# Optimization experiments

Measured on AMD Instinct MI355X. Metric: run time of the kernel, lower is better.

The kernel has to match this reference:

```python
import jax, jax.numpy as jnp
import numpy as np

NEAR, FAR, N_SAMPLES = 0.5, 2.5, 64


def setup_inputs() -> dict:
    key = jax.random.key(0)
    ks = jax.random.split(key, 12)
    N = 4096
    W = 256  # MLP width
    inp = {
        "rays_o": jax.random.normal(ks[0], (N, 3), jnp.float32),
        "rays_d": jax.random.normal(ks[1], (N, 3), jnp.float32),
        "t_rand": jax.random.uniform(ks[2], (N, N_SAMPLES), jnp.float32),
        "W1": jax.random.normal(ks[3], (3, W), jnp.float32) * 0.5,
        "b1": jnp.zeros((W,), jnp.float32),
        "W2": jax.random.normal(ks[4], (W, W), jnp.float32) * (1.0 / np.sqrt(W)),
        "b2": jnp.zeros((W,), jnp.float32),
        "W3": jax.random.normal(ks[5], (W, W), jnp.float32) * (1.0 / np.sqrt(W)),
        "b3": jnp.zeros((W,), jnp.float32),
        "Wd": jax.random.normal(ks[6], (W, 1), jnp.float32) * (1.0 / np.sqrt(W)),
        "bd": jnp.zeros((1,), jnp.float32),
        "W4": jax.random.normal(ks[7], (W + 3, 128), jnp.float32) * (1.0 / np.sqrt(W + 3)),
        "b4": jnp.zeros((128,), jnp.float32),
        "W5": jax.random.normal(ks[8], (128, 3), jnp.float32) * (1.0 / np.sqrt(128)),
        "b5": jnp.zeros((3,), jnp.float32),
    }
    return inp


def _nerf_mlp(pts, viewdirs, W1, b1, W2, b2, W3, b3, Wd, bd, W4, b4, W5, b5):
    # pts, viewdirs: [N, S, 3] -> rgb [N, S, 3], density [N, S]
    h = jax.nn.relu(pts @ W1 + b1)
    h = jax.nn.relu(h @ W2 + b2)
    h = jax.nn.relu(h @ W3 + b3)
    density = (h @ Wd + bd)[..., 0]
    h2 = jax.nn.relu(jnp.concatenate([h, viewdirs], axis=-1) @ W4 + b4)
    rgb = jax.nn.sigmoid(h2 @ W5 + b5)
    return rgb, density


def reference(rays_o, rays_d, t_rand, W1, b1, W2, b2, W3, b3, Wd, bd, W4, b4, W5, b5):
    N = rays_o.shape[0]
    # Stratified sampling along rays
    t_vals = jnp.linspace(0.0, 1.0, N_SAMPLES, dtype=jnp.float32)
    z = NEAR * (1.0 - t_vals) + FAR * t_vals                      # [S]
    z_vals = jnp.broadcast_to(z, (N, N_SAMPLES))
    mids = 0.5 * (z_vals[:, 1:] + z_vals[:, :-1])
    upper = jnp.concatenate([mids, z_vals[:, -1:]], axis=-1)
    lower = jnp.concatenate([z_vals[:, :1], mids], axis=-1)
    z_vals = lower + (upper - lower) * t_rand                      # [N, S]

    pts = rays_o[:, None, :] + rays_d[:, None, :] * z_vals[..., None]  # [N, S, 3]
    viewdirs = rays_d / (jnp.linalg.norm(rays_d, axis=-1, keepdims=True) + 1e-8)
    vdirs = jnp.broadcast_to(viewdirs[:, None, :], pts.shape)

    rgb, density = _nerf_mlp(pts, vdirs, W1, b1, W2, b2, W3, b3, Wd, bd, W4, b4, W5, b5)

    # Alpha compositing
    dists = z_vals[:, 1:] - z_vals[:, :-1]
    dists = jnp.concatenate([dists, jnp.full_like(dists[:, :1], 1e10)], axis=-1)
    alpha = 1.0 - jnp.exp(-jax.nn.relu(density) * dists)           # [N, S]
    trans = jnp.cumprod(
        jnp.concatenate([jnp.ones_like(alpha[:, :1]), 1.0 - alpha[:, :-1] + 1e-10], axis=-1),
        axis=-1,
    )
    weights = alpha * trans                                        # [N, S]
    rgb_map = jnp.sum(weights[..., None] * rgb, axis=-2)           # [N, 3]
    depth_map = jnp.sum(weights * z_vals, axis=-1)                 # [N]
    acc_map = jnp.sum(weights, axis=-1)                            # [N]
    rgb_map = rgb_map + (1.0 - acc_map[..., None])  # white background
    return rgb_map, depth_map, acc_map
```

## Files before the change

### kernel.cpp

```cpp
#include <hip/hip_runtime.h>
#include <stdint.h>


#define NRAYS 4096

typedef unsigned short u16;
typedef __attribute__((ext_vector_type(8))) short short8;
typedef __attribute__((ext_vector_type(4))) float f32x4;
typedef __attribute__((ext_vector_type(4))) unsigned int uint32x4;

__device__ __forceinline__ u16 f2bf(float f) {
  union { float f; uint32_t i; } v; v.f = f;
  return (u16)((v.i + 0x7FFFu + ((v.i >> 16) & 1u)) >> 16);
}
__device__ __forceinline__ float bf2f(u16 u) {
  union { uint32_t i; float f; } v; v.i = ((uint32_t)u) << 16; return v.f;
}
__device__ __forceinline__ uint32_t cvtpk(float lo, float hi) {
  uint32_t r;
  asm("v_cvt_pk_bf16_f32 %0, %1, %2" : "=v"(r) : "v"(lo), "v"(hi));
  return r;
}

__device__ __forceinline__ int fragidx(int n, int k) {
  return ((((n >> 4) * 8 + (k >> 5)) * 64 + ((k >> 3) & 3) * 16 + (n & 15)) << 3) + (k & 7);
}

__global__ void pack_weights(const float* __restrict__ W2, const float* __restrict__ W3,
                             const float* __restrict__ W4, u16* __restrict__ ws) {
  int idx = blockIdx.x * 256 + threadIdx.x;
  float v;
  int dst;
  if (idx < 65536) {
    int k = idx >> 8, n = idx & 255;
    v = W2[idx];
    dst = fragidx(n, k);
  } else if (idx < 131072) {
    int o = idx - 65536, k = o >> 8, n = o & 255;
    v = W3[o];
    dst = 65536 + fragidx(n, k);
  } else {
    int o = idx - 131072, k = o >> 7, n = o & 127;
    v = W4[o];
    dst = 131072 + fragidx(n, k);
  }
  ws[dst] = f2bf(v);
}

#define MFMA __builtin_amdgcn_mfma_f32_16x16x32_bf16
#define ZER4 (f32x4){0.f, 0.f, 0.f, 0.f}

#define KSTEP4(kq_, ACT) do {                                                \
    const int kq = (kq_);                                                    \
    short8 bv0 = *(const short8*)(bc0 + kq * 512);                           \
    short8 bv1 = *(const short8*)(bc1 + kq * 512);                           \
    short8 bv2 = *(const short8*)(bc2 + kq * 512);                           \
    short8 bv3 = *(const short8*)(bc3 + kq * 512);                           \
    const int sq = kq * 4 + quad;                                            \
    short8 av0 = *(const short8*)((ACT) + m0 * 256 + ((sq ^ (m0 & 31)) << 3)); \
    short8 av1 = *(const short8*)((ACT) + m1 * 256 + ((sq ^ (m1 & 31)) << 3)); \
    short8 av2 = *(const short8*)((ACT) + m2 * 256 + ((sq ^ (m2 & 31)) << 3)); \
    short8 av3 = *(const short8*)((ACT) + m3 * 256 + ((sq ^ (m3 & 31)) << 3)); \
    c00 = MFMA(av0, bv0, c00, 0, 0, 0); c10 = MFMA(av1, bv0, c10, 0, 0, 0);  \
    c20 = MFMA(av2, bv0, c20, 0, 0, 0); c30 = MFMA(av3, bv0, c30, 0, 0, 0);  \
    c01 = MFMA(av0, bv1, c01, 0, 0, 0); c11 = MFMA(av1, bv1, c11, 0, 0, 0);  \
    c21 = MFMA(av2, bv1, c21, 0, 0, 0); c31 = MFMA(av3, bv1, c31, 0, 0, 0);  \
    c02 = MFMA(av0, bv2, c02, 0, 0, 0); c12 = MFMA(av1, bv2, c12, 0, 0, 0);  \
    c22 = MFMA(av2, bv2, c22, 0, 0, 0); c32 = MFMA(av3, bv2, c32, 0, 0, 0);  \
    c03 = MFMA(av0, bv3, c03, 0, 0, 0); c13 = MFMA(av1, bv3, c13, 0, 0, 0);  \
    c23 = MFMA(av2, bv3, c23, 0, 0, 0); c33 = MFMA(av3, bv3, c33, 0, 0, 0);  \
  } while (0)

#define KSTEP2(kq_, ACT) do {                                                \
    const int kq = (kq_);                                                    \
    short8 bv0 = *(const short8*)(bc0 + kq * 512);                           \
    short8 bv1 = *(const short8*)(bc1 + kq * 512);                           \
    const int sq = kq * 4 + quad;                                            \
    short8 av0 = *(const short8*)((ACT) + m0 * 256 + ((sq ^ (m0 & 31)) << 3)); \
    short8 av1 = *(const short8*)((ACT) + m1 * 256 + ((sq ^ (m1 & 31)) << 3)); \
    short8 av2 = *(const short8*)((ACT) + m2 * 256 + ((sq ^ (m2 & 31)) << 3)); \
    short8 av3 = *(const short8*)((ACT) + m3 * 256 + ((sq ^ (m3 & 31)) << 3)); \
    c00 = MFMA(av0, bv0, c00, 0, 0, 0); c10 = MFMA(av1, bv0, c10, 0, 0, 0);  \
    c20 = MFMA(av2, bv0, c20, 0, 0, 0); c30 = MFMA(av3, bv0, c30, 0, 0, 0);  \
    c01 = MFMA(av0, bv1, c01, 0, 0, 0); c11 = MFMA(av1, bv1, c11, 0, 0, 0);  \
    c21 = MFMA(av2, bv1, c21, 0, 0, 0); c31 = MFMA(av3, bv1, c31, 0, 0, 0);  \
  } while (0)

#define EPIC(CV, mt, ng, addv, ACT) do {                                     \
    int su_ = ((ng) >> 3), so_ = ((ng) & 7);                                 \
    float f0_ = fmaxf((CV)[0] + (addv), 0.f);                                \
    float f1_ = fmaxf((CV)[1] + (addv), 0.f);                                \
    float f2_ = fmaxf((CV)[2] + (addv), 0.f);                                \
    float f3_ = fmaxf((CV)[3] + (addv), 0.f);                                \
    uint32_t p01_ = cvtpk(f0_, f1_), p23_ = cvtpk(f2_, f3_);                 \
    int mmb_ = (mt) * 16 + quad * 4;                                         \
    (ACT)[(mmb_ + 0) * 256 + ((su_ ^ ((mmb_ + 0) & 31)) << 3) + so_] = (u16)p01_;         \
    (ACT)[(mmb_ + 1) * 256 + ((su_ ^ ((mmb_ + 1) & 31)) << 3) + so_] = (u16)(p01_ >> 16); \
    (ACT)[(mmb_ + 2) * 256 + ((su_ ^ ((mmb_ + 2) & 31)) << 3) + so_] = (u16)p23_;         \
    (ACT)[(mmb_ + 3) * 256 + ((su_ ^ ((mmb_ + 3) & 31)) << 3) + so_] = (u16)(p23_ >> 16); \
  } while (0)

#define EPICD(CV, mt, ng, addv, wdv, ACT) do {                               \
    int su_ = ((ng) >> 3), so_ = ((ng) & 7);                                 \
    float f0_ = fmaxf((CV)[0] + (addv), 0.f);                                \
    float f1_ = fmaxf((CV)[1] + (addv), 0.f);                                \
    float f2_ = fmaxf((CV)[2] + (addv), 0.f);                                \
    float f3_ = fmaxf((CV)[3] + (addv), 0.f);                                \
    dp[(mt) * 4 + 0] += f0_ * (wdv);                                         \
    dp[(mt) * 4 + 1] += f1_ * (wdv);                                         \
    dp[(mt) * 4 + 2] += f2_ * (wdv);                                         \
    dp[(mt) * 4 + 3] += f3_ * (wdv);                                         \
    uint32_t p01_ = cvtpk(f0_, f1_), p23_ = cvtpk(f2_, f3_);                 \
    int mmb_ = (mt) * 16 + quad * 4;                                         \
    (ACT)[(mmb_ + 0) * 256 + ((su_ ^ ((mmb_ + 0) & 31)) << 3) + so_] = (u16)p01_;         \
    (ACT)[(mmb_ + 1) * 256 + ((su_ ^ ((mmb_ + 1) & 31)) << 3) + so_] = (u16)(p01_ >> 16); \
    (ACT)[(mmb_ + 2) * 256 + ((su_ ^ ((mmb_ + 2) & 31)) << 3) + so_] = (u16)p23_;         \
    (ACT)[(mmb_ + 3) * 256 + ((su_ ^ ((mmb_ + 3) & 31)) << 3) + so_] = (u16)(p23_ >> 16); \
  } while (0)

__global__ void __launch_bounds__(256, 2) nerf_fused(
    const float* __restrict__ rays_o, const float* __restrict__ rays_d,
    const float* __restrict__ t_rand,
    const float* __restrict__ W1, const float* __restrict__ b1,
    const float* __restrict__ b2, const float* __restrict__ b3,
    const float* __restrict__ Wd, const float* __restrict__ bd,
    const float* __restrict__ W4, const float* __restrict__ b4,
    const float* __restrict__ W5, const float* __restrict__ b5,
    const u16* __restrict__ wpack, float* __restrict__ out) {
  __shared__ u16   actA[64 * 256];
  __shared__ u16   actB[64 * 256];
  __shared__ float w1L[1040];
  __shared__ float zv[64];
  __shared__ float dist[64];
  __shared__ float dens[64];
  __shared__ float rgbL[64 * 4];
  __shared__ float vdirL[4];
  __shared__ float w5L[384];
  __shared__ float b5L[4];

  const int t = threadIdx.x;
  const int lane = t & 63;
  const int wv = t >> 6;
  const int quad = lane >> 4;
  const int l15 = lane & 15;
  const int ray = blockIdx.x;
  const int m0 = l15, m1 = l15 + 16, m2 = l15 + 32, m3 = l15 + 48;

  if (t < 64) {
    int j = t;
    float fj = (float)j;
    float zj = 0.5f + 2.0f * (fj / 63.0f);
    float lower = (j == 0)  ? zj : 0.5f * (zj + (0.5f + 2.0f * ((fj - 1.0f) / 63.0f)));
    float upper = (j == 63) ? zj : 0.5f * (zj + (0.5f + 2.0f * ((fj + 1.0f) / 63.0f)));
    float tr = t_rand[ray * 64 + j];
    zv[j] = lower + (upper - lower) * tr;
    dens[j] = 0.f;
  } else {
    int idx = t - 64;
    w5L[idx] = W5[idx];
    w5L[idx + 192] = W5[idx + 192];
  }
  {
    int base = (t + (t >> 6)) * 4;
    w1L[base + 0] = W1[t];
    w1L[base + 1] = W1[256 + t];
    w1L[base + 2] = W1[512 + t];
    w1L[base + 3] = b1[t];
  }
  if (t < 3) b5L[t] = b5[t];
  if (t == 3) b5L[3] = bd[0];
  if (t == 0) {
    float dx = rays_d[ray * 3 + 0];
    float dy = rays_d[ray * 3 + 1];
    float dz = rays_d[ray * 3 + 2];
    float nrm = sqrtf(dx * dx + dy * dy + dz * dz) + 1e-8f;
    vdirL[0] = dx / nrm; vdirL[1] = dy / nrm; vdirL[2] = dz / nrm;
  }
  __syncthreads();

  if (t < 64) dist[t] = (t < 63) ? (zv[t + 1] - zv[t]) : 1e10f;

  {
    int m = t >> 2, p = t & 3;
    float zm = zv[m];
    float px = rays_o[ray * 3 + 0] + rays_d[ray * 3 + 0] * zm;
    float py = rays_o[ray * 3 + 1] + rays_d[ray * 3 + 1] * zm;
    float pz = rays_o[ray * 3 + 2] + rays_d[ray * 3 + 2] * zm;
#pragma unroll 1
    for (int kk = 0; kk < 64; kk += 8) {
      float r[8];
#pragma unroll
      for (int j = 0; j < 8; j++) {
        int k = p * 64 + kk + j;
        f32x4 w = *(const f32x4*)(w1L + (k + p) * 4);
        r[j] = fmaxf(w[3] + px * w[0] + py * w[1] + pz * w[2], 0.f);
      }
      uint32x4 pk;
      pk[0] = cvtpk(r[0], r[1]);
      pk[1] = cvtpk(r[2], r[3]);
      pk[2] = cvtpk(r[4], r[5]);
      pk[3] = cvtpk(r[6], r[7]);
      int k0 = p * 64 + kk;
      int u = (k0 >> 3) ^ (m & 31);
      *(uint32x4*)(actA + m * 256 + u * 8) = pk;
    }
  }
  __syncthreads();

  {
    const u16* bc0 = wpack + (wv * 4 + 0) * 4096 + lane * 8;
    const u16* bc1 = wpack + (wv * 4 + 1) * 4096 + lane * 8;
    const u16* bc2 = wpack + (wv * 4 + 2) * 4096 + lane * 8;
    const u16* bc3 = wpack + (wv * 4 + 3) * 4096 + lane * 8;
    f32x4 c00 = ZER4, c01 = ZER4, c02 = ZER4, c03 = ZER4;
    f32x4 c10 = ZER4, c11 = ZER4, c12 = ZER4, c13 = ZER4;
    f32x4 c20 = ZER4, c21 = ZER4, c22 = ZER4, c23 = ZER4;
    f32x4 c30 = ZER4, c31 = ZER4, c32 = ZER4, c33 = ZER4;
#pragma unroll
    for (int kc = 0; kc < 8; kc++) KSTEP4(kc, actA);
    int ng0 = wv * 64 + l15;
    float bi0 = b2[ng0], bi1 = b2[ng0 + 16], bi2 = b2[ng0 + 32], bi3 = b2[ng0 + 48];
    EPIC(c00, 0, ng0, bi0, actB); EPIC(c10, 1, ng0, bi0, actB);
    EPIC(c20, 2, ng0, bi0, actB); EPIC(c30, 3, ng0, bi0, actB);
    EPIC(c01, 0, ng0 + 16, bi1, actB); EPIC(c11, 1, ng0 + 16, bi1, actB);
    EPIC(c21, 2, ng0 + 16, bi1, actB); EPIC(c31, 3, ng0 + 16, bi1, actB);
    EPIC(c02, 0, ng0 + 32, bi2, actB); EPIC(c12, 1, ng0 + 32, bi2, actB);
    EPIC(c22, 2, ng0 + 32, bi2, actB); EPIC(c32, 3, ng0 + 32, bi2, actB);
    EPIC(c03, 0, ng0 + 48, bi3, actB); EPIC(c13, 1, ng0 + 48, bi3, actB);
    EPIC(c23, 2, ng0 + 48, bi3, actB); EPIC(c33, 3, ng0 + 48, bi3, actB);
  }
  __syncthreads();

  {
    const u16* wB = wpack + 65536;
    const u16* bc0 = wB + (wv * 4 + 0) * 4096 + lane * 8;
    const u16* bc1 = wB + (wv * 4 + 1) * 4096 + lane * 8;
    const u16* bc2 = wB + (wv * 4 + 2) * 4096 + lane * 8;
    const u16* bc3 = wB + (wv * 4 + 3) * 4096 + lane * 8;
    f32x4 c00 = ZER4, c01 = ZER4, c02 = ZER4, c03 = ZER4;
    f32x4 c10 = ZER4, c11 = ZER4, c12 = ZER4, c13 = ZER4;
    f32x4 c20 = ZER4, c21 = ZER4, c22 = ZER4, c23 = ZER4;
    f32x4 c30 = ZER4, c31 = ZER4, c32 = ZER4, c33 = ZER4;
#pragma unroll
    for (int kc = 0; kc < 8; kc++) KSTEP4(kc, actB);
    int ng0 = wv * 64 + l15;
    float bi0 = b3[ng0], bi1 = b3[ng0 + 16], bi2 = b3[ng0 + 32], bi3 = b3[ng0 + 48];
    float wd0 = Wd[ng0], wd1 = Wd[ng0 + 16], wd2 = Wd[ng0 + 32], wd3 = Wd[ng0 + 48];
    float dp[16];
#pragma unroll
    for (int i = 0; i < 16; i++) dp[i] = 0.f;
    EPICD(c00, 0, ng0, bi0, wd0, actA); EPICD(c10, 1, ng0, bi0, wd0, actA);
    EPICD(c20, 2, ng0, bi0, wd0, actA); EPICD(c30, 3, ng0, bi0, wd0, actA);
    EPICD(c01, 0, ng0 + 16, bi1, wd1, actA); EPICD(c11, 1, ng0 + 16, bi1, wd1, actA);
    EPICD(c21, 2, ng0 + 16, bi1, wd1, actA); EPICD(c31, 3, ng0 + 16, bi1, wd1, actA);
    EPICD(c02, 0, ng0 + 32, bi2, wd2, actA); EPICD(c12, 1, ng0 + 32, bi2, wd2, actA);
    EPICD(c22, 2, ng0 + 32, bi2, wd2, actA); EPICD(c32, 3, ng0 + 32, bi2, wd2, actA);
    EPICD(c03, 0, ng0 + 48, bi3, wd3, actA); EPICD(c13, 1, ng0 + 48, bi3, wd3, actA);
    EPICD(c23, 2, ng0 + 48, bi3, wd3, actA); EPICD(c33, 3, ng0 + 48, bi3, wd3, actA);
#pragma unroll
    for (int i = 0; i < 16; i++) {
      float v = dp[i];
      v += __shfl_xor(v, 1);
      v += __shfl_xor(v, 2);
      v += __shfl_xor(v, 4);
      v += __shfl_xor(v, 8);
      dp[i] = v;
    }
    if (l15 == 0) {
#pragma unroll
      for (int i = 0; i < 16; i++) {
        int row = (i >> 2) * 16 + quad * 4 + (i & 3);
        atomicAdd(&dens[row], dp[i]);
      }
    }
  }
  __syncthreads();

  {
    const u16* wB = wpack + 131072;
    const u16* bc0 = wB + (wv * 2 + 0) * 4096 + lane * 8;
    const u16* bc1 = wB + (wv * 2 + 1) * 4096 + lane * 8;
    f32x4 c00 = ZER4, c01 = ZER4;
    f32x4 c10 = ZER4, c11 = ZER4;
    f32x4 c20 = ZER4, c21 = ZER4;
    f32x4 c30 = ZER4, c31 = ZER4;
#pragma unroll
    for (int kc = 0; kc < 8; kc++) KSTEP2(kc, actA);
    float v0 = vdirL[0], v1 = vdirL[1], v2 = vdirL[2];
    int ng0 = wv * 32 + l15;
    float ad0 = b4[ng0] + v0 * W4[32768 + ng0] + v1 * W4[32896 + ng0] + v2 * W4[33024 + ng0];
    int ng1 = ng0 + 16;
    float ad1 = b4[ng1] + v0 * W4[32768 + ng1] + v1 * W4[32896 + ng1] + v2 * W4[33024 + ng1];
    EPIC(c00, 0, ng0, ad0, actB); EPIC(c10, 1, ng0, ad0, actB);
    EPIC(c20, 2, ng0, ad0, actB); EPIC(c30, 3, ng0, ad0, actB);
    EPIC(c01, 0, ng1, ad1, actB); EPIC(c11, 1, ng1, ad1, actB);
    EPIC(c21, 2, ng1, ad1, actB); EPIC(c31, 3, ng1, ad1, actB);
  }
  __syncthreads();

  {
    int m = t >> 2, p = t & 3;
    float s0 = 0.f, s1 = 0.f, s2 = 0.f;
#pragma unroll
    for (int kk = 0; kk < 32; kk += 8) {
      int k0 = p * 32 + kk;
      short8 h = *(const short8*)(actB + m * 256 + (((k0 >> 3) ^ (m & 31)) << 3));
#pragma unroll
      for (int j = 0; j < 8; j++) {
        float hv = bf2f((u16)h[j]);
        int k = k0 + j;
        s0 += hv * w5L[k * 3 + 0];
        s1 += hv * w5L[k * 3 + 1];
        s2 += hv * w5L[k * 3 + 2];
      }
    }
    s0 += __shfl_xor(s0, 1); s0 += __shfl_xor(s0, 2);
    s1 += __shfl_xor(s1, 1); s1 += __shfl_xor(s1, 2);
    s2 += __shfl_xor(s2, 1); s2 += __shfl_xor(s2, 2);
    if (p == 0) {
      rgbL[m * 4 + 0] = 1.f / (1.f + __expf(-(s0 + b5L[0])));
      rgbL[m * 4 + 1] = 1.f / (1.f + __expf(-(s1 + b5L[1])));
      rgbL[m * 4 + 2] = 1.f / (1.f + __expf(-(s2 + b5L[2])));
    }
  }
  __syncthreads();

  if (t < 64) {
    int j = t;
    float alpha = 1.f - __expf(-fmaxf(dens[j] + b5L[3], 0.f) * dist[j]);
    float v = 1.f - alpha + 1e-10f;
    float pscan = v;
#pragma unroll
    for (int d = 1; d < 64; d <<= 1) {
      float o = __shfl_up(pscan, d);
      if (j >= d) pscan *= o;
    }
    float T = __shfl_up(pscan, 1);
    if (j == 0) T = 1.f;
    float w = alpha * T;
    float r0 = w * rgbL[j * 4 + 0];
    float r1 = w * rgbL[j * 4 + 1];
    float r2 = w * rgbL[j * 4 + 2];
    float dp = w * zv[j];
    float ac = w;
#pragma unroll
    for (int d = 32; d; d >>= 1) {
      r0 += __shfl_down(r0, d);
      r1 += __shfl_down(r1, d);
      r2 += __shfl_down(r2, d);
      dp += __shfl_down(dp, d);
      ac += __shfl_down(ac, d);
    }
    if (j == 0) {
      float bg = 1.f - ac;
      out[ray * 3 + 0] = r0 + bg;
      out[ray * 3 + 1] = r1 + bg;
      out[ray * 3 + 2] = r2 + bg;
      out[NRAYS * 3 + ray] = dp;
      out[NRAYS * 4 + ray] = ac;
    }
  }
}

extern "C" void kernel_launch(void* const* d_in, const int* in_sizes, int n_in,
                              void* d_out, int out_size, void* d_ws, size_t ws_size,
                              hipStream_t stream) {
  const float* rays_o = (const float*)d_in[0];
  const float* rays_d = (const float*)d_in[1];
  const float* t_rand = (const float*)d_in[2];
  const float* W1 = (const float*)d_in[3];
  const float* b1 = (const float*)d_in[4];
  const float* W2 = (const float*)d_in[5];
  const float* b2 = (const float*)d_in[6];
  const float* W3 = (const float*)d_in[7];
  const float* b3 = (const float*)d_in[8];
  const float* Wd = (const float*)d_in[9];
  const float* bd = (const float*)d_in[10];
  const float* W4 = (const float*)d_in[11];
  const float* b4 = (const float*)d_in[12];
  const float* W5 = (const float*)d_in[13];
  const float* b5 = (const float*)d_in[14];
  u16* wpack = (u16*)d_ws;
  float* out = (float*)d_out;

  pack_weights<<<640, 256, 0, stream>>>(W2, W3, W4, wpack);
  nerf_fused<<<NRAYS, 256, 0, stream>>>(rays_o, rays_d, t_rand, W1, b1, b2, b3,
                                        Wd, bd, W4, b4, W5, b5, wpack, out);
}
```

Before: 232.5 us.

## Move density and RGB heads onto MFMA and prefetch weight fragments into registers

```diff
diff --git a/kernel.cpp b/kernel.cpp
--- a/kernel.cpp
+++ b/kernel.cpp
@@ -27,7 +27,8 @@
 }
 
 __global__ void pack_weights(const float* __restrict__ W2, const float* __restrict__ W3,
-                             const float* __restrict__ W4, u16* __restrict__ ws) {
+                             const float* __restrict__ W4, const float* __restrict__ Wd,
+                             const float* __restrict__ W5, u16* __restrict__ ws) {
   int idx = blockIdx.x * 256 + threadIdx.x;
   float v;
   int dst;
@@ -39,10 +40,18 @@
     int o = idx - 65536, k = o >> 8, n = o & 255;
     v = W3[o];
     dst = 65536 + fragidx(n, k);
-  } else {
+  } else if (idx < 163840) {
     int o = idx - 131072, k = o >> 7, n = o & 127;
     v = W4[o];
     dst = 131072 + fragidx(n, k);
+  } else if (idx < 167936) {
+    int o = idx - 163840, k = o >> 4, n = o & 15;
+    v = (n == 0) ? Wd[k] : 0.f;
+    dst = 163840 + fragidx(n, k);
+  } else {
+    int o = idx - 167936, k = o >> 4, n = o & 15;
+    v = (n < 3) ? W5[k * 3 + n] : 0.f;
+    dst = 167936 + fragidx(n, k);
   }
   ws[dst] = f2bf(v);
 }
@@ -50,40 +59,21 @@
 #define MFMA __builtin_amdgcn_mfma_f32_16x16x32_bf16
 #define ZER4 (f32x4){0.f, 0.f, 0.f, 0.f}
 
-#define KSTEP4(kq_, ACT) do {                                                \
-    const int kq = (kq_);                                                    \
-    short8 bv0 = *(const short8*)(bc0 + kq * 512);                           \
-    short8 bv1 = *(const short8*)(bc1 + kq * 512);                           \
-    short8 bv2 = *(const short8*)(bc2 + kq * 512);                           \
-    short8 bv3 = *(const short8*)(bc3 + kq * 512);                           \
-    const int sq = kq * 4 + quad;                                            \
-    short8 av0 = *(const short8*)((ACT) + m0 * 256 + ((sq ^ (m0 & 31)) << 3)); \
-    short8 av1 = *(const short8*)((ACT) + m1 * 256 + ((sq ^ (m1 & 31)) << 3)); \
-    short8 av2 = *(const short8*)((ACT) + m2 * 256 + ((sq ^ (m2 & 31)) << 3)); \
-    short8 av3 = *(const short8*)((ACT) + m3 * 256 + ((sq ^ (m3 & 31)) << 3)); \
-    c00 = MFMA(av0, bv0, c00, 0, 0, 0); c10 = MFMA(av1, bv0, c10, 0, 0, 0);  \
-    c20 = MFMA(av2, bv0, c20, 0, 0, 0); c30 = MFMA(av3, bv0, c30, 0, 0, 0);  \
-    c01 = MFMA(av0, bv1, c01, 0, 0, 0); c11 = MFMA(av1, bv1, c11, 0, 0, 0);  \
-    c21 = MFMA(av2, bv1, c21, 0, 0, 0); c31 = MFMA(av3, bv1, c31, 0, 0, 0);  \
-    c02 = MFMA(av0, bv2, c02, 0, 0, 0); c12 = MFMA(av1, bv2, c12, 0, 0, 0);  \
-    c22 = MFMA(av2, bv2, c22, 0, 0, 0); c32 = MFMA(av3, bv2, c32, 0, 0, 0);  \
-    c03 = MFMA(av0, bv3, c03, 0, 0, 0); c13 = MFMA(av1, bv3, c13, 0, 0, 0);  \
-    c23 = MFMA(av2, bv3, c23, 0, 0, 0); c33 = MFMA(av3, bv3, c33, 0, 0, 0);  \
-  } while (0)
-
-#define KSTEP2(kq_, ACT) do {                                                \
-    const int kq = (kq_);                                                    \
-    short8 bv0 = *(const short8*)(bc0 + kq * 512);                           \
-    short8 bv1 = *(const short8*)(bc1 + kq * 512);                           \
-    const int sq = kq * 4 + quad;                                            \
-    short8 av0 = *(const short8*)((ACT) + m0 * 256 + ((sq ^ (m0 & 31)) << 3)); \
-    short8 av1 = *(const short8*)((ACT) + m1 * 256 + ((sq ^ (m1 & 31)) << 3)); \
-    short8 av2 = *(const short8*)((ACT) + m2 * 256 + ((sq ^ (m2 & 31)) << 3)); \
-    short8 av3 = *(const short8*)((ACT) + m3 * 256 + ((sq ^ (m3 & 31)) << 3)); \
-    c00 = MFMA(av0, bv0, c00, 0, 0, 0); c10 = MFMA(av1, bv0, c10, 0, 0, 0);  \
-    c20 = MFMA(av2, bv0, c20, 0, 0, 0); c30 = MFMA(av3, bv0, c30, 0, 0, 0);  \
-    c01 = MFMA(av0, bv1, c01, 0, 0, 0); c11 = MFMA(av1, bv1, c11, 0, 0, 0);  \
-    c21 = MFMA(av2, bv1, c21, 0, 0, 0); c31 = MFMA(av3, bv1, c31, 0, 0, 0);  \
+#define LDA4(ACT, SQ)                                                          \
+    short8 av0 = *(const short8*)((ACT) + m0 * 256 + (((SQ) ^ (m0 & 31)) << 3)); \
+    short8 av1 = *(const short8*)((ACT) + m1 * 256 + (((SQ) ^ (m1 & 31)) << 3)); \
+    short8 av2 = *(const short8*)((ACT) + m2 * 256 + (((SQ) ^ (m2 & 31)) << 3)); \
+    short8 av3 = *(const short8*)((ACT) + m3 * 256 + (((SQ) ^ (m3 & 31)) << 3))
+
+#define MF16v(B0, B1, B2_, B3_) do {                                         \
+    c00 = MFMA(av0, B0, c00, 0, 0, 0); c10 = MFMA(av1, B0, c10, 0, 0, 0);    \
+    c20 = MFMA(av2, B0, c20, 0, 0, 0); c30 = MFMA(av3, B0, c30, 0, 0, 0);    \
+    c01 = MFMA(av0, B1, c01, 0, 0, 0); c11 = MFMA(av1, B1, c11, 0, 0, 0);    \
+    c21 = MFMA(av2, B1, c21, 0, 0, 0); c31 = MFMA(av3, B1, c31, 0, 0, 0);    \
+    c02 = MFMA(av0, B2_, c02, 0, 0, 0); c12 = MFMA(av1, B2_, c12, 0, 0, 0);  \
+    c22 = MFMA(av2, B2_, c22, 0, 0, 0); c32 = MFMA(av3, B2_, c32, 0, 0, 0);  \
+    c03 = MFMA(av0, B3_, c03, 0, 0, 0); c13 = MFMA(av1, B3_, c13, 0, 0, 0);  \
+    c23 = MFMA(av2, B3_, c23, 0, 0, 0); c33 = MFMA(av3, B3_, c33, 0, 0, 0);  \
   } while (0)
 
 #define EPIC(CV, mt, ng, addv, ACT) do {                                     \
@@ -100,32 +90,14 @@
     (ACT)[(mmb_ + 3) * 256 + ((su_ ^ ((mmb_ + 3) & 31)) << 3) + so_] = (u16)(p23_ >> 16); \
   } while (0)
 
-#define EPICD(CV, mt, ng, addv, wdv, ACT) do {                               \
-    int su_ = ((ng) >> 3), so_ = ((ng) & 7);                                 \
-    float f0_ = fmaxf((CV)[0] + (addv), 0.f);                                \
-    float f1_ = fmaxf((CV)[1] + (addv), 0.f);                                \
-    float f2_ = fmaxf((CV)[2] + (addv), 0.f);                                \
-    float f3_ = fmaxf((CV)[3] + (addv), 0.f);                                \
-    dp[(mt) * 4 + 0] += f0_ * (wdv);                                         \
-    dp[(mt) * 4 + 1] += f1_ * (wdv);                                         \
-    dp[(mt) * 4 + 2] += f2_ * (wdv);                                         \
-    dp[(mt) * 4 + 3] += f3_ * (wdv);                                         \
-    uint32_t p01_ = cvtpk(f0_, f1_), p23_ = cvtpk(f2_, f3_);                 \
-    int mmb_ = (mt) * 16 + quad * 4;                                         \
-    (ACT)[(mmb_ + 0) * 256 + ((su_ ^ ((mmb_ + 0) & 31)) << 3) + so_] = (u16)p01_;         \
-    (ACT)[(mmb_ + 1) * 256 + ((su_ ^ ((mmb_ + 1) & 31)) << 3) + so_] = (u16)(p01_ >> 16); \
-    (ACT)[(mmb_ + 2) * 256 + ((su_ ^ ((mmb_ + 2) & 31)) << 3) + so_] = (u16)p23_;         \
-    (ACT)[(mmb_ + 3) * 256 + ((su_ ^ ((mmb_ + 3) & 31)) << 3) + so_] = (u16)(p23_ >> 16); \
-  } while (0)
-
 __global__ void __launch_bounds__(256, 2) nerf_fused(
     const float* __restrict__ rays_o, const float* __restrict__ rays_d,
     const float* __restrict__ t_rand,
     const float* __restrict__ W1, const float* __restrict__ b1,
     const float* __restrict__ b2, const float* __restrict__ b3,
-    const float* __restrict__ Wd, const float* __restrict__ bd,
+    const float* __restrict__ bd,
     const float* __restrict__ W4, const float* __restrict__ b4,
-    const float* __restrict__ W5, const float* __restrict__ b5,
+    const float* __restrict__ b5,
     const u16* __restrict__ wpack, float* __restrict__ out) {
   __shared__ u16   actA[64 * 256];
   __shared__ u16   actB[64 * 256];
@@ -135,7 +107,6 @@
   __shared__ float dens[64];
   __shared__ float rgbL[64 * 4];
   __shared__ float vdirL[4];
-  __shared__ float w5L[384];
   __shared__ float b5L[4];
 
   const int t = threadIdx.x;
@@ -145,6 +116,21 @@
   const int l15 = lane & 15;
   const int ray = blockIdx.x;
   const int m0 = l15, m1 = l15 + 16, m2 = l15 + 32, m3 = l15 + 48;
+
+  short8 B2a[8], B2b[8], B2c[8], B2d[8];
+  {
+    const u16* q0 = wpack + (wv * 4 + 0) * 4096 + lane * 8;
+    const u16* q1 = wpack + (wv * 4 + 1) * 4096 + lane * 8;
+    const u16* q2 = wpack + (wv * 4 + 2) * 4096 + lane * 8;
+    const u16* q3 = wpack + (wv * 4 + 3) * 4096 + lane * 8;
+#pragma unroll
+    for (int kq = 0; kq < 8; kq++) {
+      B2a[kq] = *(const short8*)(q0 + kq * 512);
+      B2b[kq] = *(const short8*)(q1 + kq * 512);
+      B2c[kq] = *(const short8*)(q2 + kq * 512);
+      B2d[kq] = *(const short8*)(q3 + kq * 512);
+    }
+  }
 
   if (t < 64) {
     int j = t;
@@ -154,11 +140,6 @@
     float upper = (j == 63) ? zj : 0.5f * (zj + (0.5f + 2.0f * ((fj + 1.0f) / 63.0f)));
     float tr = t_rand[ray * 64 + j];
     zv[j] = lower + (upper - lower) * tr;
-    dens[j] = 0.f;
-  } else {
-    int idx = t - 64;
-    w5L[idx] = W5[idx];
-    w5L[idx + 192] = W5[idx + 192];
   }
   {
     int base = (t + (t >> 6)) * 4;
@@ -207,19 +188,33 @@
   }
   __syncthreads();
 
-  {
-    const u16* bc0 = wpack + (wv * 4 + 0) * 4096 + lane * 8;
-    const u16* bc1 = wpack + (wv * 4 + 1) * 4096 + lane * 8;
-    const u16* bc2 = wpack + (wv * 4 + 2) * 4096 + lane * 8;
-    const u16* bc3 = wpack + (wv * 4 + 3) * 4096 + lane * 8;
+  short8 B3a[4], B3b[4], B3c[4], B3d[4];
+
+  {
+    int ng0 = wv * 64 + l15;
+    float bi0 = b2[ng0], bi1 = b2[ng0 + 16], bi2 = b2[ng0 + 32], bi3 = b2[ng0 + 48];
     f32x4 c00 = ZER4, c01 = ZER4, c02 = ZER4, c03 = ZER4;
     f32x4 c10 = ZER4, c11 = ZER4, c12 = ZER4, c13 = ZER4;
     f32x4 c20 = ZER4, c21 = ZER4, c22 = ZER4, c23 = ZER4;
     f32x4 c30 = ZER4, c31 = ZER4, c32 = ZER4, c33 = ZER4;
 #pragma unroll
-    for (int kc = 0; kc < 8; kc++) KSTEP4(kc, actA);
-    int ng0 = wv * 64 + l15;
-    float bi0 = b2[ng0], bi1 = b2[ng0 + 16], bi2 = b2[ng0 + 32], bi3 = b2[ng0 + 48];
+    for (int kq = 0; kq < 8; kq++) {
+      LDA4(actA, kq * 4 + quad);
+      MF16v(B2a[kq], B2b[kq], B2c[kq], B2d[kq]);
+    }
+    {
+      const u16* r0 = wpack + 65536 + (wv * 4 + 0) * 4096 + lane * 8;
+      const u16* r1 = wpack + 65536 + (wv * 4 + 1) * 4096 + lane * 8;
+      const u16* r2 = wpack + 65536 + (wv * 4 + 2) * 4096 + lane * 8;
+      const u16* r3 = wpack + 65536 + (wv * 4 + 3) * 4096 + lane * 8;
+#pragma unroll
+      for (int kq = 0; kq < 4; kq++) {
+        B3a[kq] = *(const short8*)(r0 + kq * 512);
+        B3b[kq] = *(const short8*)(r1 + kq * 512);
+        B3c[kq] = *(const short8*)(r2 + kq * 512);
+        B3d[kq] = *(const short8*)(r3 + kq * 512);
+      }
+    }
     EPIC(c00, 0, ng0, bi0, actB); EPIC(c10, 1, ng0, bi0, actB);
     EPIC(c20, 2, ng0, bi0, actB); EPIC(c30, 3, ng0, bi0, actB);
     EPIC(c01, 0, ng0 + 16, bi1, actB); EPIC(c11, 1, ng0 + 16, bi1, actB);
@@ -231,96 +226,118 @@
   }
   __syncthreads();
 
-  {
-    const u16* wB = wpack + 65536;
-    const u16* bc0 = wB + (wv * 4 + 0) * 4096 + lane * 8;
-    const u16* bc1 = wB + (wv * 4 + 1) * 4096 + lane * 8;
-    const u16* bc2 = wB + (wv * 4 + 2) * 4096 + lane * 8;
-    const u16* bc3 = wB + (wv * 4 + 3) * 4096 + lane * 8;
+  short8 L4a[2], L4b[2], L4d[2];
+
+  {
+    int ng0 = wv * 64 + l15;
+    float bi0 = b3[ng0], bi1 = b3[ng0 + 16], bi2 = b3[ng0 + 32], bi3 = b3[ng0 + 48];
+    const u16* r0 = wpack + 65536 + (wv * 4 + 0) * 4096 + lane * 8;
+    const u16* r1 = wpack + 65536 + (wv * 4 + 1) * 4096 + lane * 8;
+    const u16* r2 = wpack + 65536 + (wv * 4 + 2) * 4096 + lane * 8;
+    const u16* r3 = wpack + 65536 + (wv * 4 + 3) * 4096 + lane * 8;
     f32x4 c00 = ZER4, c01 = ZER4, c02 = ZER4, c03 = ZER4;
     f32x4 c10 = ZER4, c11 = ZER4, c12 = ZER4, c13 = ZER4;
     f32x4 c20 = ZER4, c21 = ZER4, c22 = ZER4, c23 = ZER4;
     f32x4 c30 = ZER4, c31 = ZER4, c32 = ZER4, c33 = ZER4;
 #pragma unroll
-    for (int kc = 0; kc < 8; kc++) KSTEP4(kc, actB);
-    int ng0 = wv * 64 + l15;
-    float bi0 = b3[ng0], bi1 = b3[ng0 + 16], bi2 = b3[ng0 + 32], bi3 = b3[ng0 + 48];
-    float wd0 = Wd[ng0], wd1 = Wd[ng0 + 16], wd2 = Wd[ng0 + 32], wd3 = Wd[ng0 + 48];
-    float dp[16];
-#pragma unroll
-    for (int i = 0; i < 16; i++) dp[i] = 0.f;
-    EPICD(c00, 0, ng0, bi0, wd0, actA); EPICD(c10, 1, ng0, bi0, wd0, actA);
-    EPICD(c20, 2, ng0, bi0, wd0, actA); EPICD(c30, 3, ng0, bi0, wd0, actA);
-    EPICD(c01, 0, ng0 + 16, bi1, wd1, actA); EPICD(c11, 1, ng0 + 16, bi1, wd1, actA);
-    EPICD(c21, 2, ng0 + 16, bi1, wd1, actA); EPICD(c31, 3, ng0 + 16, bi1, wd1, actA);
-    EPICD(c02, 0, ng0 + 32, bi2, wd2, actA); EPICD(c12, 1, ng0 + 32, bi2, wd2, actA);
-    EPICD(c22, 2, ng0 + 32, bi2, wd2, actA); EPICD(c32, 3, ng0 + 32, bi2, wd2, actA);
-    EPICD(c03, 0, ng0 + 48, bi3, wd3, actA); EPICD(c13, 1, ng0 + 48, bi3, wd3, actA);
-    EPICD(c23, 2, ng0 + 48, bi3, wd3, actA); EPICD(c33, 3, ng0 + 48, bi3, wd3, actA);
-#pragma unroll
-    for (int i = 0; i < 16; i++) {
-      float v = dp[i];
-      v += __shfl_xor(v, 1);
-      v += __shfl_xor(v, 2);
-      v += __shfl_xor(v, 4);
-      v += __shfl_xor(v, 8);
-      dp[i] = v;
-    }
-    if (l15 == 0) {
-#pragma unroll
-      for (int i = 0; i < 16; i++) {
-        int row = (i >> 2) * 16 + quad * 4 + (i & 3);
-        atomicAdd(&dens[row], dp[i]);
-      }
-    }
-  }
-  __syncthreads();
-
-  {
-    const u16* wB = wpack + 131072;
-    const u16* bc0 = wB + (wv * 2 + 0) * 4096 + lane * 8;
-    const u16* bc1 = wB + (wv * 2 + 1) * 4096 + lane * 8;
+    for (int kq = 0; kq < 8; kq++) {
+      short8 b0, b1v, b2v, b3v;
+      if (kq < 4) { b0 = B3a[kq]; b1v = B3b[kq]; b2v = B3c[kq]; b3v = B3d[kq]; }
+      else {
+        b0 = *(const short8*)(r0 + kq * 512);
+        b1v = *(const short8*)(r1 + kq * 512);
+        b2v = *(const short8*)(r2 + kq * 512);
+        b3v = *(const short8*)(r3 + kq * 512);
+      }
+      LDA4(actB, kq * 4 + quad);
+      MF16v(b0, b1v, b2v, b3v);
+    }
+    {
+      const u16* s0 = wpack + 131072 + (wv * 2 + 0) * 4096 + lane * 8;
+      const u16* s1 = wpack + 131072 + (wv * 2 + 1) * 4096 + lane * 8;
+      const u16* sD = wpack + 163840 + lane * 8;
+#pragma unroll
+      for (int kq = 0; kq < 2; kq++) {
+        L4a[kq] = *(const short8*)(s0 + kq * 512);
+        L4b[kq] = *(const short8*)(s1 + kq * 512);
+        L4d[kq] = *(const short8*)(sD + kq * 512);
+      }
+    }
+    EPIC(c00, 0, ng0, bi0, actA); EPIC(c10, 1, ng0, bi0, actA);
+    EPIC(c20, 2, ng0, bi0, actA); EPIC(c30, 3, ng0, bi0, actA);
+    EPIC(c01, 0, ng0 + 16, bi1, actA); EPIC(c11, 1, ng0 + 16, bi1, actA);
+    EPIC(c21, 2, ng0 + 16, bi1, actA); EPIC(c31, 3, ng0 + 16, bi1, actA);
+    EPIC(c02, 0, ng0 + 32, bi2, actA); EPIC(c12, 1, ng0 + 32, bi2, actA);
+    EPIC(c22, 2, ng0 + 32, bi2, actA); EPIC(c32, 3, ng0 + 32, bi2, actA);
+    EPIC(c03, 0, ng0 + 48, bi3, actA); EPIC(c13, 1, ng0 + 48, bi3, actA);
+    EPIC(c23, 2, ng0 + 48, bi3, actA); EPIC(c33, 3, ng0 + 48, bi3, actA);
+  }
+  __syncthreads();
+
+  short8 W5f[4];
+
+  {
+    float v0 = vdirL[0], v1 = vdirL[1], v2 = vdirL[2];
+    int ng0 = wv * 32 + l15;
+    int ng1 = ng0 + 16;
+    float ad0 = b4[ng0] + v0 * W4[32768 + ng0] + v1 * W4[32896 + ng0] + v2 * W4[33024 + ng0];
+    float ad1 = b4[ng1] + v0 * W4[32768 + ng1] + v1 * W4[32896 + ng1] + v2 * W4[33024 + ng1];
+    const u16* s0 = wpack + 131072 + (wv * 2 + 0) * 4096 + lane * 8;
+    const u16* s1 = wpack + 131072 + (wv * 2 + 1) * 4096 + lane * 8;
+    const u16* sD = wpack + 163840 + lane * 8;
     f32x4 c00 = ZER4, c01 = ZER4;
     f32x4 c10 = ZER4, c11 = ZER4;
     f32x4 c20 = ZER4, c21 = ZER4;
     f32x4 c30 = ZER4, c31 = ZER4;
-#pragma unroll
-    for (int kc = 0; kc < 8; kc++) KSTEP2(kc, actA);
-    float v0 = vdirL[0], v1 = vdirL[1], v2 = vdirL[2];
-    int ng0 = wv * 32 + l15;
-    float ad0 = b4[ng0] + v0 * W4[32768 + ng0] + v1 * W4[32896 + ng0] + v2 * W4[33024 + ng0];
-    int ng1 = ng0 + 16;
-    float ad1 = b4[ng1] + v0 * W4[32768 + ng1] + v1 * W4[32896 + ng1] + v2 * W4[33024 + ng1];
+    f32x4 c40 = ZER4, c41 = ZER4, c42 = ZER4, c43 = ZER4;
+#pragma unroll
+    for (int kq = 0; kq < 8; kq++) {
+      short8 b0 = (kq < 2) ? L4a[kq] : *(const short8*)(s0 + kq * 512);
+      short8 b1v = (kq < 2) ? L4b[kq] : *(const short8*)(s1 + kq * 512);
+      short8 bD = (kq < 2) ? L4d[kq] : *(const short8*)(sD + kq * 512);
+      LDA4(actA, kq * 4 + quad);
+      c00 = MFMA(av0, b0, c00, 0, 0, 0); c10 = MFMA(av1, b0, c10, 0, 0, 0);
+      c20 = MFMA(av2, b0, c20, 0, 0, 0); c30 = MFMA(av3, b0, c30, 0, 0, 0);
+      c01 = MFMA(av0, b1v, c01, 0, 0, 0); c11 = MFMA(av1, b1v, c11, 0, 0, 0);
+      c21 = MFMA(av2, b1v, c21, 0, 0, 0); c31 = MFMA(av3, b1v, c31, 0, 0, 0);
+      c40 = MFMA(av0, bD, c40, 0, 0, 0); c41 = MFMA(av1, bD, c41, 0, 0, 0);
+      c42 = MFMA(av2, bD, c42, 0, 0, 0); c43 = MFMA(av3, bD, c43, 0, 0, 0);
+    }
+    {
+      const u16* s5 = wpack + 167936 + lane * 8;
+#pragma unroll
+      for (int kq = 0; kq < 4; kq++) W5f[kq] = *(const short8*)(s5 + kq * 512);
+    }
     EPIC(c00, 0, ng0, ad0, actB); EPIC(c10, 1, ng0, ad0, actB);
     EPIC(c20, 2, ng0, ad0, actB); EPIC(c30, 3, ng0, ad0, actB);
     EPIC(c01, 0, ng1, ad1, actB); EPIC(c11, 1, ng1, ad1, actB);
     EPIC(c21, 2, ng1, ad1, actB); EPIC(c31, 3, ng1, ad1, actB);
-  }
-  __syncthreads();
-
-  {
-    int m = t >> 2, p = t & 3;
-    float s0 = 0.f, s1 = 0.f, s2 = 0.f;
-#pragma unroll
-    for (int kk = 0; kk < 32; kk += 8) {
-      int k0 = p * 32 + kk;
-      short8 h = *(const short8*)(actB + m * 256 + (((k0 >> 3) ^ (m & 31)) << 3));
-#pragma unroll
-      for (int j = 0; j < 8; j++) {
-        float hv = bf2f((u16)h[j]);
-        int k = k0 + j;
-        s0 += hv * w5L[k * 3 + 0];
-        s1 += hv * w5L[k * 3 + 1];
-        s2 += hv * w5L[k * 3 + 2];
-      }
-    }
-    s0 += __shfl_xor(s0, 1); s0 += __shfl_xor(s0, 2);
-    s1 += __shfl_xor(s1, 1); s1 += __shfl_xor(s1, 2);
-    s2 += __shfl_xor(s2, 1); s2 += __shfl_xor(s2, 2);
-    if (p == 0) {
-      rgbL[m * 4 + 0] = 1.f / (1.f + __expf(-(s0 + b5L[0])));
-      rgbL[m * 4 + 1] = 1.f / (1.f + __expf(-(s1 + b5L[1])));
-      rgbL[m * 4 + 2] = 1.f / (1.f + __expf(-(s2 + b5L[2])));
+    if (wv == 0 && l15 == 0) {
+#pragma unroll
+      for (int r = 0; r < 4; r++) {
+        dens[ 0 + quad * 4 + r] = c40[r];
+        dens[16 + quad * 4 + r] = c41[r];
+        dens[32 + quad * 4 + r] = c42[r];
+        dens[48 + quad * 4 + r] = c43[r];
+      }
+    }
+  }
+  __syncthreads();
+
+  {
+    int mR = wv * 16 + l15;
+    f32x4 cR = ZER4;
+#pragma unroll
+    for (int kq = 0; kq < 4; kq++) {
+      short8 av = *(const short8*)(actB + mR * 256 + (((kq * 4 + quad) ^ (mR & 31)) << 3));
+      cR = MFMA(av, W5f[kq], cR, 0, 0, 0);
+    }
+    if (l15 < 3) {
+#pragma unroll
+      for (int r = 0; r < 4; r++) {
+        int row = wv * 16 + quad * 4 + r;
+        rgbL[row * 4 + l15] = 1.f / (1.f + __expf(-(cR[r] + b5L[l15])));
+      }
     }
   }
   __syncthreads();
@@ -383,7 +400,7 @@
   u16* wpack = (u16*)d_ws;
   float* out = (float*)d_out;
 
-  pack_weights<<<640, 256, 0, stream>>>(W2, W3, W4, wpack);
+  pack_weights<<<664, 256, 0, stream>>>(W2, W3, W4, Wd, W5, wpack);
   nerf_fused<<<NRAYS, 256, 0, stream>>>(rays_o, rays_d, t_rand, W1, b1, b2, b3,
-                                        Wd, bd, W4, b4, W5, b5, wpack, out);
-}
+                                        bd, W4, b4, b5, wpack, out);
+}
```

After: 216.9 us (median of 2 runs). 1.07x faster.
